# Kernel tuning notes

Measured on AMD Instinct MI355X. Metric: run time of the kernel, lower is better.

The kernel has to match this reference:

```python
import jax, jax.numpy as jnp
from jax import lax
import numpy as np

B, T, F = 4, 2048, 128
DM, L, STRIDE, KF = 512, 4, 4, 2
N, DC, E = 16, 4, 2
DI = E * DM          # 1024 inner dim
R = (DM + 15) // 16  # 32 dt_rank
K = KF * STRIDE      # 8 front conv kernel
EPS = 1e-5

def _ln(x, w, b):
    m = x.mean(-1, keepdims=True)
    v = ((x - m) ** 2).mean(-1, keepdims=True)
    return (x - m) / jnp.sqrt(v + EPS) * w + b

def _causal_dwconv(x, w, b):
    # x: (B,Ts,DI), w: (DI,DC) depthwise causal conv
    xc = x.transpose(0, 2, 1)
    y = lax.conv_general_dilated(xc, w[:, None, :], (1,), [(DC - 1, 0)],
                                 feature_group_count=w.shape[0])
    return (y + b[None, :, None]).transpose(0, 2, 1)

def _selective_scan(dt, A, Bm, Cm, u):
    # dt,u: (B,Ts,DI); A: (DI,N); Bm,Cm: (B,Ts,N)
    dA = jnp.exp(dt[..., None] * A)                  # (B,Ts,DI,N)
    dBu = (dt * u)[..., None] * Bm[:, :, None, :]    # (B,Ts,DI,N)
    def step(h, inp):
        dA_t, dBu_t, C_t = inp
        h = dA_t * h + dBu_t
        y = jnp.einsum('bdn,bn->bd', h, C_t)
        return h, y
    h0 = jnp.zeros((u.shape[0], DI, N), u.dtype)
    _, ys = lax.scan(step, h0, (dA.transpose(1, 0, 2, 3),
                                dBu.transpose(1, 0, 2, 3),
                                Cm.transpose(1, 0, 2)))
    return ys.transpose(1, 0, 2)

def _mamba(x, in_w, cw, cb, xp_w, dtp_w, dtp_b, A_log, Dp, out_w):
    xz = jnp.einsum('btd,ed->bte', x, in_w)          # (B,Ts,2*DI)
    xi, z = jnp.split(xz, 2, axis=-1)
    xi = jax.nn.silu(_causal_dwconv(xi, cw, cb))
    x_dbl = jnp.einsum('btd,ed->bte', xi, xp_w)      # (B,Ts,R+2N)
    dt, Bm, Cm = jnp.split(x_dbl, [R, R + N], axis=-1)
    dt = jax.nn.softplus(jnp.einsum('btr,dr->btd', dt, dtp_w) + dtp_b)
    y = _selective_scan(dt, -jnp.exp(A_log), Bm, Cm, xi)
    y = (y + xi * Dp) * jax.nn.silu(z)
    return jnp.einsum('btd,od->bto', y, out_w)

def _forward(x, conv_w, conv_b, in_proj_w, conv1d_w, conv1d_b, x_proj_w,
             dt_proj_w, dt_proj_b, A_log, D_skip, ln_w, ln_b, out_proj_w,
             norm_w, norm_b):
    T_orig = x.shape[1]
    # causal strided front conv: pad (K-1,0), stride=STRIDE, then GELU
    h = lax.conv_general_dilated(x.transpose(0, 2, 1), conv_w, (STRIDE,),
                                 [(K - 1, 0)])
    h = jax.nn.gelu((h + conv_b[None, :, None]).transpose(0, 2, 1),
                    approximate=False)               # (B,T//STRIDE,DM)
    for l in range(L):
        hn = _ln(h, ln_w[l], ln_b[l])
        h = h + _mamba(hn, in_proj_w[l], conv1d_w[l], conv1d_b[l],
                       x_proj_w[l], dt_proj_w[l], dt_proj_b[l],
                       A_log[l], D_skip[l], out_proj_w[l])
    h = _ln(h, norm_w, norm_b)
    # repeat_interleave upsample back to original resolution
    return jnp.repeat(h, STRIDE, axis=1)[:, :T_orig, :]

def setup_inputs():
    key = jax.random.key(0)
    ks = jax.random.split(key, 8)
    g = lambda i, shape, s=0.02: jax.random.normal(ks[i], shape, jnp.float32) * s
    A_log = jnp.tile(jnp.log(jnp.arange(1, N + 1, dtype=jnp.float32)), (L, DI, 1))
    return dict(
        x=jax.random.normal(ks[0], (B, T, F), jnp.float32),
        conv_w=g(1, (DM, F, K)), conv_b=jnp.zeros((DM,), jnp.float32),
        in_proj_w=g(2, (L, 2 * DI, DM)),
        conv1d_w=g(3, (L, DI, DC), 0.2),
        conv1d_b=jnp.zeros((L, DI), jnp.float32),
        x_proj_w=g(4, (L, R + 2 * N, DI)),
        dt_proj_w=g(5, (L, DI, R), 0.1),
        dt_proj_b=jnp.full((L, DI), -2.0, jnp.float32),
        A_log=A_log,
        D_skip=jnp.ones((L, DI), jnp.float32),
        ln_w=jnp.ones((L, DM), jnp.float32),
        ln_b=jnp.zeros((L, DM), jnp.float32),
        out_proj_w=g(6, (L, DM, DI)),
        norm_w=jnp.ones((DM,), jnp.float32),
        norm_b=jnp.zeros((DM,), jnp.float32),
    )

def reference(x, conv_w, conv_b, in_proj_w, conv1d_w, conv1d_b, x_proj_w,
              dt_proj_w, dt_proj_b, A_log, D_skip, ln_w, ln_b, out_proj_w,
              norm_w, norm_b):
    return _forward(x, conv_w, conv_b, in_proj_w, conv1d_w, conv1d_b, x_proj_w,
                    dt_proj_w, dt_proj_b, A_log, D_skip, ln_w, ln_b, out_proj_w,
                    norm_w, norm_b)
```

## Files before the change

### kernel.cpp

```cpp
#include <hip/hip_runtime.h>
#include <hip/hip_bf16.h>

typedef unsigned short u16;
typedef u16 u16x8 __attribute__((ext_vector_type(8)));
typedef __bf16 bf16x8 __attribute__((ext_vector_type(8)));
typedef float f32x4 __attribute__((ext_vector_type(4)));

#define GLOAD16(gsrc, ldst) \
  __builtin_amdgcn_global_load_lds((const __attribute__((address_space(1))) void*)(gsrc), \
                                   (__attribute__((address_space(3))) void*)(ldst), 16, 0, 0)

__device__ __forceinline__ u16 f2bf(float f) {
  union { float f; unsigned u; } c; c.f = f;
  unsigned r = c.u + 0x7FFFu + ((c.u >> 16) & 1u);
  return (u16)(r >> 16);
}
__device__ __forceinline__ float bf2f(u16 v) {
  union { unsigned u; float f; } c; c.u = ((unsigned)v) << 16;
  return c.f;
}

__global__ __launch_bounds__(256) void cast_weights_k(
    const float* __restrict__ in_w, const float* __restrict__ xp_w,
    const float* __restrict__ out_w, const float* __restrict__ conv_w,
    const float* __restrict__ A_log, const float* __restrict__ c1w,
    u16* __restrict__ winb, u16* __restrict__ wxpb, u16* __restrict__ woutb,
    u16* __restrict__ wconvb, float* __restrict__ Apre, float* __restrict__ cwt) {
  int i = blockIdx.x * 256 + threadIdx.x;
  if (i < 1048576) {
    const float4 v = *(const float4*)(in_w + (size_t)i * 4);
    ushort2 lo = {f2bf(v.x), f2bf(v.y)}, hi = {f2bf(v.z), f2bf(v.w)};
    *(ushort2*)(winb + (size_t)i * 4) = lo;
    *(ushort2*)(winb + (size_t)i * 4 + 2) = hi;
    return;
  }
  i -= 1048576;
  if (i < 65536) {
    const float4 v = *(const float4*)(xp_w + (size_t)i * 4);
    ushort2 lo = {f2bf(v.x), f2bf(v.y)}, hi = {f2bf(v.z), f2bf(v.w)};
    *(ushort2*)(wxpb + (size_t)i * 4) = lo;
    *(ushort2*)(wxpb + (size_t)i * 4 + 2) = hi;
    return;
  }
  i -= 65536;
  if (i < 524288) {
    const float4 v = *(const float4*)(out_w + (size_t)i * 4);
    ushort2 lo = {f2bf(v.x), f2bf(v.y)}, hi = {f2bf(v.z), f2bf(v.w)};
    *(ushort2*)(woutb + (size_t)i * 4) = lo;
    *(ushort2*)(woutb + (size_t)i * 4 + 2) = hi;
    return;
  }
  i -= 524288;
  if (i < 131072) {
    const int m = i >> 8, r = (i & 255) * 4;
    const int kk = r >> 7, ff = r & 127;
    const float* src = conv_w + m * 1024 + kk;
    ushort2 lo = {f2bf(src[(ff + 0) * 8]), f2bf(src[(ff + 1) * 8])};
    ushort2 hi = {f2bf(src[(ff + 2) * 8]), f2bf(src[(ff + 3) * 8])};
    *(ushort2*)(wconvb + (size_t)i * 4) = lo;
    *(ushort2*)(wconvb + (size_t)i * 4 + 2) = hi;
    return;
  }
  i -= 131072;
  if (i < 16384) {
    const float4 v = *(const float4*)(A_log + (size_t)i * 4);
    float4 o;
    o.x = -__expf(v.x); o.y = -__expf(v.y); o.z = -__expf(v.z); o.w = -__expf(v.w);
    *(float4*)(Apre + (size_t)i * 4) = o;
    return;
  }
  i -= 16384;
  if (i < 4096) {
    const int og = i * 4, l = og >> 12, r = og & 4095;
    const int j = r >> 10, d0 = r & 1023;
    float4 o;
    o.x = c1w[l * 4096 + (d0 + 0) * 4 + j];
    o.y = c1w[l * 4096 + (d0 + 1) * 4 + j];
    o.z = c1w[l * 4096 + (d0 + 2) * 4 + j];
    o.w = c1w[l * 4096 + (d0 + 3) * 4 + j];
    *(float4*)(cwt + (size_t)i * 4) = o;
  }
}

__global__ __launch_bounds__(256) void im2col_k(const float* __restrict__ x,
                                                u16* __restrict__ xc) {
  const int i = blockIdx.x * 256 + threadIdx.x;
  const int col = (i & 255) * 4, tok = i >> 8;
  const int kk = col >> 7, ff = col & 127;
  const int b = tok >> 9, to = tok & 511;
  const int t = to * 4 + kk - 7;
  float4 v = {0.f, 0.f, 0.f, 0.f};
  if (t >= 0) v = *(const float4*)(x + ((size_t)b * 2048 + t) * 128 + ff);
  ushort2 lo = {f2bf(v.x), f2bf(v.y)}, hi = {f2bf(v.z), f2bf(v.w)};
  *(ushort2*)(xc + (size_t)i * 4) = lo;
  *(ushort2*)(xc + (size_t)i * 4 + 2) = hi;
}

template <int NW>
__global__ __launch_bounds__(NW * 64) void gemm2_k(
    const u16* __restrict__ A, int lda, const u16* __restrict__ Bw, int ldb,
    u16* __restrict__ C, int ldc, int Ks, size_t mn) {
  __shared__ __align__(16) char smem[NW * 16384];
  const int tid = threadIdx.x, lane = tid & 63, wid = tid >> 6;
  const int bm = blockIdx.x, bn = blockIdx.y;
  const int Kw = Ks / NW;
  const size_t koff = (size_t)blockIdx.z * Ks + (size_t)wid * Kw;
  char* base = smem + wid * 16384;
  const int srow = lane >> 2, sslot = lane & 3;
  const int nk = Kw >> 5;
  f32x4 acc[4][4] = {};

  auto stage = [&](int buf, int kt) {
#pragma unroll
    for (int c = 0; c < 8; ++c) {
      int lrow, gr, ldx; const u16* src;
      if (c < 4) { lrow = c * 16 + srow; gr = bm * 64 + lrow; src = A; ldx = lda; }
      else { lrow = (c - 4) * 16 + srow; gr = bn * 64 + lrow; src = Bw; ldx = ldb; }
      const int slot = sslot ^ ((lrow >> 1) & 3);
      GLOAD16(src + (size_t)gr * ldx + koff + kt * 32 + slot * 8,
              base + buf * 8192 + c * 1024);
    }
  };

  stage(0, 0);
  if (nk > 1) stage(1, 1);
  const int s = lane >> 4, r0 = lane & 15;
  for (int kt = 0; kt < nk; ++kt) {
    const int p = kt & 1;
    if (kt + 1 < nk) asm volatile("s_waitcnt vmcnt(8)" ::: "memory");
    else             asm volatile("s_waitcnt vmcnt(0)" ::: "memory");
    __builtin_amdgcn_sched_barrier(0);
    bf16x8 af[4], bfv[4];
#pragma unroll
    for (int i = 0; i < 4; ++i) {
      const int r = i * 16 + r0;
      af[i] = *(const bf16x8*)(base + p * 8192 + r * 64 + ((s ^ ((r >> 1) & 3)) << 4));
      bfv[i] = *(const bf16x8*)(base + p * 8192 + 4096 + r * 64 + ((s ^ ((r >> 1) & 3)) << 4));
    }
    asm volatile("s_waitcnt lgkmcnt(0)" ::: "memory");
    __builtin_amdgcn_sched_barrier(0);
    if (kt + 2 < nk) stage(p, kt + 2);
#pragma unroll
    for (int mi = 0; mi < 4; ++mi)
#pragma unroll
      for (int ni = 0; ni < 4; ++ni)
        acc[mi][ni] = __builtin_amdgcn_mfma_f32_16x16x32_bf16(af[mi], bfv[ni],
                                                              acc[mi][ni], 0, 0, 0);
    __builtin_amdgcn_sched_barrier(0);
  }
  if constexpr (NW == 2) {
    if (wid == 1) {
      f32x4* dst = (f32x4*)(smem + 16384);
#pragma unroll
      for (int mi = 0; mi < 4; ++mi)
#pragma unroll
        for (int ni = 0; ni < 4; ++ni)
          dst[(mi * 4 + ni) * 64 + lane] = acc[mi][ni];
    }
    __syncthreads();
    if (wid == 1) return;
    const f32x4* src1 = (const f32x4*)(smem + 16384);
#pragma unroll
    for (int mi = 0; mi < 4; ++mi)
#pragma unroll
      for (int ni = 0; ni < 4; ++ni)
        acc[mi][ni] += src1[(mi * 4 + ni) * 64 + lane];
  }
  const int er0 = lane & 15, eg4 = lane >> 4;
  u16* Cz = C + (size_t)blockIdx.z * mn;
#pragma unroll
  for (int mi = 0; mi < 4; ++mi)
#pragma unroll
    for (int ni = 0; ni < 4; ++ni) {
      const int col = bn * 64 + ni * 16 + er0;
#pragma unroll
      for (int r = 0; r < 4; ++r) {
        const int row = bm * 64 + mi * 16 + eg4 * 4 + r;
        Cz[(size_t)row * ldc + col] = f2bf(acc[mi][ni][r]);
      }
    }
}

template <int MODE>
__global__ __launch_bounds__(256) void red_ln_k(
    const u16* __restrict__ P, float* __restrict__ h,
    const float* __restrict__ bias, const float* __restrict__ w,
    const float* __restrict__ bb, u16* __restrict__ o, float* __restrict__ oup) {
  const int row = blockIdx.x * 4 + (threadIdx.x >> 6);
  const int lane = threadIdx.x & 63;
  const size_t base = (size_t)row * 512 + lane * 8;
  float v[8];
  if constexpr (MODE == 0) {
#pragma unroll
    for (int j = 0; j < 8; ++j) v[j] = 0.f;
  } else {
    float4 a = *(const float4*)(h + base);
    float4 b4 = *(const float4*)(h + base + 4);
    v[0] = a.x; v[1] = a.y; v[2] = a.z; v[3] = a.w;
    v[4] = b4.x; v[5] = b4.y; v[6] = b4.z; v[7] = b4.w;
  }
#pragma unroll
  for (int s2 = 0; s2 < 4; ++s2) {
    const u16x8 pv = *(const u16x8*)(P + (size_t)s2 * 1048576 + base);
#pragma unroll
    for (int j = 0; j < 8; ++j) v[j] += bf2f(pv[j]);
  }
  if constexpr (MODE == 0) {
    const int col = lane * 8;
#pragma unroll
    for (int j = 0; j < 8; ++j) {
      const float t = v[j] + bias[col + j];
      v[j] = 0.5f * t * (1.f + erff(t * 0.70710678118f));
    }
  }
  if constexpr (MODE != 2) {
    float4 oa; oa.x = v[0]; oa.y = v[1]; oa.z = v[2]; oa.w = v[3];
    float4 ob; ob.x = v[4]; ob.y = v[5]; ob.z = v[6]; ob.w = v[7];
    *(float4*)(h + base) = oa;
    *(float4*)(h + base + 4) = ob;
  }
  float s = 0.f, sq = 0.f;
#pragma unroll
  for (int j = 0; j < 8; ++j) { s += v[j]; sq += v[j] * v[j]; }
  for (int off = 32; off; off >>= 1) { s += __shfl_xor(s, off); sq += __shfl_xor(sq, off); }
  const float m = s * (1.f / 512.f);
  const float rs = rsqrtf(sq * (1.f / 512.f) - m * m + 1e-5f);
  const float* wp = w + lane * 8; const float* bp = bb + lane * 8;
  float nv[8];
#pragma unroll
  for (int j = 0; j < 8; ++j) nv[j] = (v[j] - m) * rs * wp[j] + bp[j];
  if constexpr (MODE != 2) {
    uint4 uu;
    uu.x = (unsigned)f2bf(nv[0]) | ((unsigned)f2bf(nv[1]) << 16);
    uu.y = (unsigned)f2bf(nv[2]) | ((unsigned)f2bf(nv[3]) << 16);
    uu.z = (unsigned)f2bf(nv[4]) | ((unsigned)f2bf(nv[5]) << 16);
    uu.w = (unsigned)f2bf(nv[6]) | ((unsigned)f2bf(nv[7]) << 16);
    *(uint4*)(o + base) = uu;
  } else {
    const int bi = row >> 9, t0 = row & 511;
    float4 lo; lo.x = nv[0]; lo.y = nv[1]; lo.z = nv[2]; lo.w = nv[3];
    float4 hi; hi.x = nv[4]; hi.y = nv[5]; hi.z = nv[6]; hi.w = nv[7];
    float* obp = oup + ((size_t)bi * 2048 + (size_t)t0 * 4) * 512 + lane * 8;
#pragma unroll
    for (int q = 0; q < 4; ++q) {
      *(float4*)(obp + (size_t)q * 512) = lo;
      *(float4*)(obp + (size_t)q * 512 + 4) = hi;
    }
  }
}

template <int NS>
__global__ __launch_bounds__(256) void redx_k(const u16* __restrict__ P,
                                              float* __restrict__ C) {
  const size_t i8 = ((size_t)blockIdx.x * 256 + threadIdx.x) * 8;
  if (i8 >= 131072) return;
  float v[8] = {};
#pragma unroll
  for (int s2 = 0; s2 < NS; ++s2) {
    const u16x8 pv = *(const u16x8*)(P + (size_t)s2 * 131072 + i8);
#pragma unroll
    for (int j = 0; j < 8; ++j) v[j] += bf2f(pv[j]);
  }
  float4 a; a.x = v[0]; a.y = v[1]; a.z = v[2]; a.w = v[3];
  float4 b; b.x = v[4]; b.y = v[5]; b.z = v[6]; b.w = v[7];
  *(float4*)(C + i8) = a;
  *(float4*)(C + i8 + 4) = b;
}

__global__ __launch_bounds__(256) void dtproj_k(const float* __restrict__ xdbl,
                                                const float* __restrict__ dtw,
                                                const float* __restrict__ dtbias,
                                                u16* __restrict__ dtbb) {
  __shared__ float xls[32 * 32];
  const int tid = threadIdx.x;
  const int dc = (blockIdx.x & 3) * 256;
  const int tg = (blockIdx.x >> 2) * 32;
  const int d = dc + tid;
  float4 w[8];
#pragma unroll
  for (int j = 0; j < 8; ++j) w[j] = *(const float4*)(dtw + (size_t)d * 32 + j * 4);
  for (int i = tid; i < 1024; i += 256) {
    const int t = i >> 5, r = i & 31;
    xls[i] = xdbl[(size_t)(tg + t) * 64 + r];
  }
  const float b = dtbias[d];
  __syncthreads();
  for (int t = 0; t < 32; ++t) {
    const float4* xr = (const float4*)&xls[t * 32];
    float acc = b;
#pragma unroll
    for (int j = 0; j < 8; ++j) {
      const float4 xv = xr[j];
      acc = fmaf(w[j].x, xv.x, acc); acc = fmaf(w[j].y, xv.y, acc);
      acc = fmaf(w[j].z, xv.z, acc); acc = fmaf(w[j].w, xv.w, acc);
    }
    dtbb[(size_t)(tg + t) * 1024 + d] =
        f2bf(fmaxf(acc, 0.f) + __logf(1.f + __expf(-fabsf(acc))));
  }
}

__global__ __launch_bounds__(256) void dwconv_k(const u16* __restrict__ xzb,
                                                const float* __restrict__ cwt,
                                                const float* __restrict__ cb,
                                                u16* __restrict__ xib) {
  const int i = blockIdx.x * 256 + threadIdx.x;
  const int d0 = (i & 127) * 8, tok = i >> 7, t = tok & 511;
  const u16* p = xzb + (size_t)tok * 2048 + d0;
  const float4 b0 = *(const float4*)(cb + d0);
  const float4 b1 = *(const float4*)(cb + d0 + 4);
  float acc[8] = {b0.x, b0.y, b0.z, b0.w, b1.x, b1.y, b1.z, b1.w};
#pragma unroll
  for (int j = 0; j < 4; ++j) {
    const int ts = t + j - 3;
    if (ts >= 0) {
      const u16x8 xv = *(const u16x8*)(p + (j - 3) * 2048);
      const float4 wa = *(const float4*)(cwt + j * 1024 + d0);
      const float4 wb = *(const float4*)(cwt + j * 1024 + d0 + 4);
      acc[0] = fmaf(bf2f(xv[0]), wa.x, acc[0]);
      acc[1] = fmaf(bf2f(xv[1]), wa.y, acc[1]);
      acc[2] = fmaf(bf2f(xv[2]), wa.z, acc[2]);
      acc[3] = fmaf(bf2f(xv[3]), wa.w, acc[3]);
      acc[4] = fmaf(bf2f(xv[4]), wb.x, acc[4]);
      acc[5] = fmaf(bf2f(xv[5]), wb.y, acc[5]);
      acc[6] = fmaf(bf2f(xv[6]), wb.z, acc[6]);
      acc[7] = fmaf(bf2f(xv[7]), wb.w, acc[7]);
    }
  }
  u16x8 o;
#pragma unroll
  for (int e = 0; e < 8; ++e)
    o[e] = f2bf(acc[e] / (1.f + __expf(-acc[e])));
  *(u16x8*)(xib + (size_t)i * 8) = o;
}

__global__ __launch_bounds__(256) void scan1_k(const u16* __restrict__ dtbb,
                                               const u16* __restrict__ xib,
                                               const float* __restrict__ xd,
                                               const float* __restrict__ Ap,
                                               float* __restrict__ hF,
                                               float* __restrict__ aP) {
  const int blk = blockIdx.x;
  const int d = (blk & 3) * 256 + threadIdx.x;
  const int c = (blk >> 2) & 31, b = blk >> 7;
  float A[16], h[16], ap[16];
#pragma unroll
  for (int n = 0; n < 16; ++n) { A[n] = Ap[d * 16 + n]; h[n] = 0.f; ap[n] = 1.f; }
  const int t0 = c * 16;
  for (int t = t0; t < t0 + 16; ++t) {
    const int tok = b * 512 + t;
    const float dtv = bf2f(dtbb[(size_t)tok * 1024 + d]);
    const float u = bf2f(xib[(size_t)tok * 1024 + d]);
    const float s = dtv * u;
    const float* Bp = xd + (size_t)tok * 64 + 32;
#pragma unroll
    for (int n = 0; n < 16; ++n) {
      const float dA = __expf(dtv * A[n]);
      h[n] = dA * h[n] + s * Bp[n];
      ap[n] *= dA;
    }
  }
#pragma unroll
  for (int n = 0; n < 16; ++n) {
    const size_t o = ((size_t)(b * 32 + c) * 16 + n) * 1024 + d;
    hF[o] = h[n]; aP[o] = ap[n];
  }
}

__global__ __launch_bounds__(256) void scan2_k(const float* __restrict__ hF,
                                               const float* __restrict__ aP,
                                               float* __restrict__ hI) {
  const int bi = blockIdx.x >> 6;
  const int n = (blockIdx.x >> 2) & 15;
  const int d = (blockIdx.x & 3) * 256 + threadIdx.x;
  float h = 0.f;
  for (int c = 0; c < 32; ++c) {
    const size_t o = ((size_t)((bi * 32 + c) * 16 + n)) * 1024 + d;
    hI[o] = h;
    h = fmaf(aP[o], h, hF[o]);
  }
}

__global__ __launch_bounds__(256) void scan3_k(const u16* __restrict__ dtbb,
                                               const u16* __restrict__ xib,
                                               const float* __restrict__ xd,
                                               const float* __restrict__ Ap,
                                               const float* __restrict__ hI,
                                               const u16* __restrict__ xzb,
                                               const float* __restrict__ Dp,
                                               u16* __restrict__ y2b) {
  const int blk = blockIdx.x;
  const int d = (blk & 3) * 256 + threadIdx.x;
  const int c = (blk >> 2) & 31, b = blk >> 7;
  float A[16], h[16];
#pragma unroll
  for (int n = 0; n < 16; ++n) {
    A[n] = Ap[d * 16 + n];
    h[n] = hI[((size_t)(b * 32 + c) * 16 + n) * 1024 + d];
  }
  const float Dd = Dp[d];
  const int t0 = c * 16;
  for (int t = t0; t < t0 + 16; ++t) {
    const int tok = b * 512 + t;
    const float dtv = bf2f(dtbb[(size_t)tok * 1024 + d]);
    const float u = bf2f(xib[(size_t)tok * 1024 + d]);
    const float s = dtv * u;
    const float* Bp = xd + (size_t)tok * 64 + 32;
    const float* Cp = xd + (size_t)tok * 64 + 48;
    float y = 0.f;
#pragma unroll
    for (int n = 0; n < 16; ++n) {
      const float dA = __expf(dtv * A[n]);
      h[n] = dA * h[n] + s * Bp[n];
      y = fmaf(h[n], Cp[n], y);
    }
    const float z = bf2f(xzb[(size_t)tok * 2048 + 1024 + d]);
    const float sz = z / (1.f + __expf(-z));
    y2b[(size_t)tok * 1024 + d] = f2bf((y + u * Dd) * sz);
  }
}

extern "C" void kernel_launch(void* const* d_in, const int* in_sizes, int n_in,
                              void* d_out, int out_size, void* d_ws, size_t ws_size,
                              hipStream_t stream) {
  const float* x      = (const float*)d_in[0];
  const float* conv_w = (const float*)d_in[1];
  const float* conv_b = (const float*)d_in[2];
  const float* in_w   = (const float*)d_in[3];
  const float* c1w    = (const float*)d_in[4];
  const float* c1b    = (const float*)d_in[5];
  const float* xp_w   = (const float*)d_in[6];
  const float* dt_w   = (const float*)d_in[7];
  const float* dt_b   = (const float*)d_in[8];
  const float* A_log  = (const float*)d_in[9];
  const float* D_skip = (const float*)d_in[10];
  const float* ln_w   = (const float*)d_in[11];
  const float* ln_b   = (const float*)d_in[12];
  const float* out_w  = (const float*)d_in[13];
  const float* norm_w = (const float*)d_in[14];
  const float* norm_b = (const float*)d_in[15];
  float* out = (float*)d_out;

  float* f = (float*)d_ws;
  float* h    = f; f += 1048576;
  float* xdbl = f; f += 131072;
  float* Apre = f; f += 65536;
  float* cwt  = f; f += 16384;
  float* hF   = f; f += 2097152;
  float* aP   = f; f += 2097152;
  float* hI   = f; f += 2097152;
  u16* ub = (u16*)f;
  u16* hnb    = ub; ub += 1048576;
  u16* xzb    = ub; ub += 4194304;
  u16* xib    = ub; ub += 2097152;
  u16* dtbb   = ub; ub += 2097152;
  u16* y2b    = ub; ub += 2097152;
  u16* xcolb  = ub; ub += 2097152;
  u16* pp     = ub; ub += 4194304;
  u16* ppB    = ub; ub += 1048576;
  u16* winb   = ub; ub += 4194304;
  u16* wxpb   = ub; ub += 262144;
  u16* woutb  = ub; ub += 2097152;
  u16* wconvb = ub; ub += 524288;

  cast_weights_k<<<6993, 256, 0, stream>>>(in_w, xp_w, out_w, conv_w, A_log, c1w,
                                           winb, wxpb, woutb, wconvb, Apre, cwt);
  im2col_k<<<2048, 256, 0, stream>>>(x, xcolb);
  gemm2_k<2><<<dim3(32, 8, 4), 128, 0, stream>>>(xcolb, 1024, wconvb, 1024,
                                                 pp, 512, 256, (size_t)1048576);
  red_ln_k<0><<<512, 256, 0, stream>>>(pp, h, conv_b, ln_w, ln_b, hnb, nullptr);
  for (int l = 0; l < 4; ++l) {
    gemm2_k<2><<<dim3(32, 32, 1), 128, 0, stream>>>(hnb, 512, winb + l * 1048576,
                                                    512, xzb, 2048, 512, 0);
    dwconv_k<<<1024, 256, 0, stream>>>(xzb, cwt + l * 4096, c1b + l * 1024, xib);
    gemm2_k<2><<<dim3(32, 1, 8), 128, 0, stream>>>(xib, 1024, wxpb + l * 65536,
                                                   1024, ppB, 64, 128, (size_t)131072);
    redx_k<8><<<64, 256, 0, stream>>>(ppB, xdbl);
    dtproj_k<<<256, 256, 0, stream>>>(xdbl, dt_w + l * 32768, dt_b + l * 1024, dtbb);
    scan1_k<<<512, 256, 0, stream>>>(dtbb, xib, xdbl, Apre + l * 16384, hF, aP);
    scan2_k<<<256, 256, 0, stream>>>(hF, aP, hI);
    scan3_k<<<512, 256, 0, stream>>>(dtbb, xib, xdbl, Apre + l * 16384, hI, xzb,
                                     D_skip + l * 1024, y2b);
    gemm2_k<2><<<dim3(32, 8, 4), 128, 0, stream>>>(y2b, 1024, woutb + l * 524288,
                                                   1024, pp, 512, 256, (size_t)1048576);
    if (l < 3) {
      red_ln_k<1><<<512, 256, 0, stream>>>(pp, h, nullptr, ln_w + (l + 1) * 512,
                                           ln_b + (l + 1) * 512, hnb, nullptr);
    } else {
      red_ln_k<2><<<512, 256, 0, stream>>>(pp, h, nullptr, norm_w, norm_b,
                                           nullptr, out);
    }
  }
}
```

Baseline: 346.2 us.

## Fuse im2col into weight cast, merge reduce with dt-proj, pack scan carries in bf16

The im2col conversion is folded into the weight-casting launch, and the split-K reduction of x_proj is merged with the dt projection into one kernel. This removes two launches per run, one of them inside the per-layer loop. The chunk-scan carry state (per-chunk final h and decay product) is packed into one 32-bit word as two bf16 values, and the inter-chunk prefix is stored as bf16, cutting scan traffic between the three scan kernels. The bf16 carries lower precision in the recurrent state, and every redxdt block now re-reduces the x_proj partial sums.

```diff
diff --git a/kernel.cpp b/kernel.cpp
--- a/kernel.cpp
+++ b/kernel.cpp
@@ -24,8 +24,10 @@
     const float* __restrict__ in_w, const float* __restrict__ xp_w,
     const float* __restrict__ out_w, const float* __restrict__ conv_w,
     const float* __restrict__ A_log, const float* __restrict__ c1w,
+    const float* __restrict__ x,
     u16* __restrict__ winb, u16* __restrict__ wxpb, u16* __restrict__ woutb,
-    u16* __restrict__ wconvb, float* __restrict__ Apre, float* __restrict__ cwt) {
+    u16* __restrict__ wconvb, float* __restrict__ Apre, float* __restrict__ cwt,
+    u16* __restrict__ xcolb) {
   int i = blockIdx.x * 256 + threadIdx.x;
   if (i < 1048576) {
     const float4 v = *(const float4*)(in_w + (size_t)i * 4);
@@ -79,21 +81,20 @@
     o.z = c1w[l * 4096 + (d0 + 2) * 4 + j];
     o.w = c1w[l * 4096 + (d0 + 3) * 4 + j];
     *(float4*)(cwt + (size_t)i * 4) = o;
-  }
-}
-
-__global__ __launch_bounds__(256) void im2col_k(const float* __restrict__ x,
-                                                u16* __restrict__ xc) {
-  const int i = blockIdx.x * 256 + threadIdx.x;
-  const int col = (i & 255) * 4, tok = i >> 8;
-  const int kk = col >> 7, ff = col & 127;
-  const int b = tok >> 9, to = tok & 511;
-  const int t = to * 4 + kk - 7;
-  float4 v = {0.f, 0.f, 0.f, 0.f};
-  if (t >= 0) v = *(const float4*)(x + ((size_t)b * 2048 + t) * 128 + ff);
-  ushort2 lo = {f2bf(v.x), f2bf(v.y)}, hi = {f2bf(v.z), f2bf(v.w)};
-  *(ushort2*)(xc + (size_t)i * 4) = lo;
-  *(ushort2*)(xc + (size_t)i * 4 + 2) = hi;
+    return;
+  }
+  i -= 4096;
+  if (i < 524288) {
+    const int col = (i & 255) * 4, tok = i >> 8;
+    const int kk = col >> 7, ff = col & 127;
+    const int b = tok >> 9, to = tok & 511;
+    const int t = to * 4 + kk - 7;
+    float4 v = {0.f, 0.f, 0.f, 0.f};
+    if (t >= 0) v = *(const float4*)(x + ((size_t)b * 2048 + t) * 128 + ff);
+    ushort2 lo = {f2bf(v.x), f2bf(v.y)}, hi = {f2bf(v.z), f2bf(v.w)};
+    *(ushort2*)(xcolb + (size_t)i * 4) = lo;
+    *(ushort2*)(xcolb + (size_t)i * 4 + 2) = hi;
+  }
 }
 
 template <int NW>
@@ -249,44 +250,30 @@
   }
 }
 
-template <int NS>
-__global__ __launch_bounds__(256) void redx_k(const u16* __restrict__ P,
-                                              float* __restrict__ C) {
-  const size_t i8 = ((size_t)blockIdx.x * 256 + threadIdx.x) * 8;
-  if (i8 >= 131072) return;
-  float v[8] = {};
-#pragma unroll
-  for (int s2 = 0; s2 < NS; ++s2) {
-    const u16x8 pv = *(const u16x8*)(P + (size_t)s2 * 131072 + i8);
-#pragma unroll
-    for (int j = 0; j < 8; ++j) v[j] += bf2f(pv[j]);
-  }
-  float4 a; a.x = v[0]; a.y = v[1]; a.z = v[2]; a.w = v[3];
-  float4 b; b.x = v[4]; b.y = v[5]; b.z = v[6]; b.w = v[7];
-  *(float4*)(C + i8) = a;
-  *(float4*)(C + i8 + 4) = b;
-}
-
-__global__ __launch_bounds__(256) void dtproj_k(const float* __restrict__ xdbl,
-                                                const float* __restrict__ dtw,
-                                                const float* __restrict__ dtbias,
-                                                u16* __restrict__ dtbb) {
-  __shared__ float xls[32 * 32];
+__global__ __launch_bounds__(256) void redxdt_k(
+    const u16* __restrict__ ppB, const float* __restrict__ dtw,
+    const float* __restrict__ dtbias, float* __restrict__ xdbl,
+    u16* __restrict__ dtbb) {
+  __shared__ float xls[32 * 64];
   const int tid = threadIdx.x;
-  const int dc = (blockIdx.x & 3) * 256;
-  const int tg = (blockIdx.x >> 2) * 32;
-  const int d = dc + tid;
+  const int tg = blockIdx.x >> 2, dblk = blockIdx.x & 3;
+  const int T0 = tg * 32;
+  for (int i = tid; i < 2048; i += 256) {
+    const size_t off = (size_t)T0 * 64 + i;
+    float v = 0.f;
+#pragma unroll
+    for (int s2 = 0; s2 < 8; ++s2) v += bf2f(ppB[(size_t)s2 * 131072 + off]);
+    xls[i] = v;
+    if (dblk == 0) xdbl[off] = v;
+  }
+  const int d = dblk * 256 + tid;
   float4 w[8];
 #pragma unroll
   for (int j = 0; j < 8; ++j) w[j] = *(const float4*)(dtw + (size_t)d * 32 + j * 4);
-  for (int i = tid; i < 1024; i += 256) {
-    const int t = i >> 5, r = i & 31;
-    xls[i] = xdbl[(size_t)(tg + t) * 64 + r];
-  }
   const float b = dtbias[d];
   __syncthreads();
   for (int t = 0; t < 32; ++t) {
-    const float4* xr = (const float4*)&xls[t * 32];
+    const float4* xr = (const float4*)&xls[t * 64];
     float acc = b;
 #pragma unroll
     for (int j = 0; j < 8; ++j) {
@@ -294,7 +281,7 @@
       acc = fmaf(w[j].x, xv.x, acc); acc = fmaf(w[j].y, xv.y, acc);
       acc = fmaf(w[j].z, xv.z, acc); acc = fmaf(w[j].w, xv.w, acc);
     }
-    dtbb[(size_t)(tg + t) * 1024 + d] =
+    dtbb[(size_t)(T0 + t) * 1024 + d] =
         f2bf(fmaxf(acc, 0.f) + __logf(1.f + __expf(-fabsf(acc))));
   }
 }
@@ -337,8 +324,7 @@
                                                const u16* __restrict__ xib,
                                                const float* __restrict__ xd,
                                                const float* __restrict__ Ap,
-                                               float* __restrict__ hF,
-                                               float* __restrict__ aP) {
+                                               unsigned* __restrict__ hA) {
   const int blk = blockIdx.x;
   const int d = (blk & 3) * 256 + threadIdx.x;
   const int c = (blk >> 2) & 31, b = blk >> 7;
@@ -362,21 +348,21 @@
 #pragma unroll
   for (int n = 0; n < 16; ++n) {
     const size_t o = ((size_t)(b * 32 + c) * 16 + n) * 1024 + d;
-    hF[o] = h[n]; aP[o] = ap[n];
-  }
-}
-
-__global__ __launch_bounds__(256) void scan2_k(const float* __restrict__ hF,
-                                               const float* __restrict__ aP,
-                                               float* __restrict__ hI) {
+    hA[o] = (unsigned)f2bf(h[n]) | ((unsigned)f2bf(ap[n]) << 16);
+  }
+}
+
+__global__ __launch_bounds__(256) void scan2_k(const unsigned* __restrict__ hA,
+                                               u16* __restrict__ hI) {
   const int bi = blockIdx.x >> 6;
   const int n = (blockIdx.x >> 2) & 15;
   const int d = (blockIdx.x & 3) * 256 + threadIdx.x;
   float h = 0.f;
   for (int c = 0; c < 32; ++c) {
     const size_t o = ((size_t)((bi * 32 + c) * 16 + n)) * 1024 + d;
-    hI[o] = h;
-    h = fmaf(aP[o], h, hF[o]);
+    hI[o] = f2bf(h);
+    const unsigned pk = hA[o];
+    h = fmaf(bf2f((u16)(pk >> 16)), h, bf2f((u16)(pk & 0xffffu)));
   }
 }
 
@@ -384,7 +370,7 @@
                                                const u16* __restrict__ xib,
                                                const float* __restrict__ xd,
                                                const float* __restrict__ Ap,
-                                               const float* __restrict__ hI,
+                                               const u16* __restrict__ hI,
                                                const u16* __restrict__ xzb,
                                                const float* __restrict__ Dp,
                                                u16* __restrict__ y2b) {
@@ -395,7 +381,7 @@
 #pragma unroll
   for (int n = 0; n < 16; ++n) {
     A[n] = Ap[d * 16 + n];
-    h[n] = hI[((size_t)(b * 32 + c) * 16 + n) * 1024 + d];
+    h[n] = bf2f(hI[((size_t)(b * 32 + c) * 16 + n) * 1024 + d]);
   }
   const float Dd = Dp[d];
   const int t0 = c * 16;
@@ -445,9 +431,7 @@
   float* xdbl = f; f += 131072;
   float* Apre = f; f += 65536;
   float* cwt  = f; f += 16384;
-  float* hF   = f; f += 2097152;
-  float* aP   = f; f += 2097152;
-  float* hI   = f; f += 2097152;
+  unsigned* hA = (unsigned*)f; f += 2097152;
   u16* ub = (u16*)f;
   u16* hnb    = ub; ub += 1048576;
   u16* xzb    = ub; ub += 4194304;
@@ -455,6 +439,7 @@
   u16* dtbb   = ub; ub += 2097152;
   u16* y2b    = ub; ub += 2097152;
   u16* xcolb  = ub; ub += 2097152;
+  u16* hIu    = ub; ub += 2097152;
   u16* pp     = ub; ub += 4194304;
   u16* ppB    = ub; ub += 1048576;
   u16* winb   = ub; ub += 4194304;
@@ -462,9 +447,9 @@
   u16* woutb  = ub; ub += 2097152;
   u16* wconvb = ub; ub += 524288;
 
-  cast_weights_k<<<6993, 256, 0, stream>>>(in_w, xp_w, out_w, conv_w, A_log, c1w,
-                                           winb, wxpb, woutb, wconvb, Apre, cwt);
-  im2col_k<<<2048, 256, 0, stream>>>(x, xcolb);
+  cast_weights_k<<<9040, 256, 0, stream>>>(in_w, xp_w, out_w, conv_w, A_log, c1w,
+                                           x, winb, wxpb, woutb, wconvb, Apre,
+                                           cwt, xcolb);
   gemm2_k<2><<<dim3(32, 8, 4), 128, 0, stream>>>(xcolb, 1024, wconvb, 1024,
                                                  pp, 512, 256, (size_t)1048576);
   red_ln_k<0><<<512, 256, 0, stream>>>(pp, h, conv_b, ln_w, ln_b, hnb, nullptr);
@@ -474,11 +459,11 @@
     dwconv_k<<<1024, 256, 0, stream>>>(xzb, cwt + l * 4096, c1b + l * 1024, xib);
     gemm2_k<2><<<dim3(32, 1, 8), 128, 0, stream>>>(xib, 1024, wxpb + l * 65536,
                                                    1024, ppB, 64, 128, (size_t)131072);
-    redx_k<8><<<64, 256, 0, stream>>>(ppB, xdbl);
-    dtproj_k<<<256, 256, 0, stream>>>(xdbl, dt_w + l * 32768, dt_b + l * 1024, dtbb);
-    scan1_k<<<512, 256, 0, stream>>>(dtbb, xib, xdbl, Apre + l * 16384, hF, aP);
-    scan2_k<<<256, 256, 0, stream>>>(hF, aP, hI);
-    scan3_k<<<512, 256, 0, stream>>>(dtbb, xib, xdbl, Apre + l * 16384, hI, xzb,
+    redxdt_k<<<256, 256, 0, stream>>>(ppB, dt_w + l * 32768, dt_b + l * 1024,
+                                      xdbl, dtbb);
+    scan1_k<<<512, 256, 0, stream>>>(dtbb, xib, xdbl, Apre + l * 16384, hA);
+    scan2_k<<<256, 256, 0, stream>>>(hA, hIu);
+    scan3_k<<<512, 256, 0, stream>>>(dtbb, xib, xdbl, Apre + l * 16384, hIu, xzb,
                                      D_skip + l * 1024, y2b);
     gemm2_k<2><<<dim3(32, 8, 4), 128, 0, stream>>>(y2b, 1024, woutb + l * 524288,
                                                    1024, pp, 512, 256, (size_t)1048576);
```

Result: no change. 346.0 us (-0.1%).
